# Performance work log

Hardware: AMD Instinct MI355X
Metric: run time of the kernel (lower is better)

The kernel has to match this reference:

```python
import jax, jax.numpy as jnp
import numpy as np

N_VOX = 100000   # active voxels
K = 27           # 3^3 kernel offsets
M = 60000        # matched (in, out) pairs per offset
CIN = 64
COUT = 64
BN_EPS = 1e-5


def setup_inputs() -> dict:
    key = jax.random.key(0)
    ks = jax.random.split(key, 6)
    feats = jax.random.normal(ks[0], (N_VOX, CIN), dtype=jnp.float32)
    W = jax.random.normal(ks[1], (K, CIN, COUT), dtype=jnp.float32) * 0.05
    gamma = jnp.ones((COUT,), dtype=jnp.float32)
    beta = jnp.zeros((COUT,), dtype=jnp.float32)
    running_mean = jax.random.normal(ks[2], (COUT,), dtype=jnp.float32) * 0.1
    running_var = jax.random.uniform(ks[3], (COUT,), dtype=jnp.float32, minval=0.5, maxval=1.5)
    in_idx = jax.random.randint(ks[4], (K, M), 0, N_VOX, dtype=jnp.int32)
    out_idx = jax.random.randint(ks[5], (K, M), 0, N_VOX, dtype=jnp.int32)
    return {
        "feats": feats, "W": W, "gamma": gamma, "beta": beta,
        "running_mean": running_mean, "running_var": running_var,
        "in_idx": in_idx, "out_idx": out_idx,
    }


def reference(feats, W, gamma, beta, running_mean, running_var, in_idx, out_idx):
    # Sparse conv as gather-GEMM-scatter over the hash-map kernel map.
    gathered = feats[in_idx]                              # [K, M, Cin]
    contrib = jnp.einsum('kmc,kcd->kmd', gathered, W)     # [K, M, Cout]
    out = jax.ops.segment_sum(
        contrib.reshape(-1, W.shape[-1]),                 # [K*M, Cout]
        out_idx.reshape(-1),
        num_segments=feats.shape[0],
    )                                                     # [N, Cout]
    # BatchNorm (inference, running stats) + ReLU
    inv = jax.lax.rsqrt(running_var + BN_EPS)
    y = (out - running_mean) * (inv * gamma) + beta
    return jnp.maximum(y, 0.0)
```

## Files before the change

kernel.cpp:

```cpp
#include <hip/hip_runtime.h>

#define N_VOX 100000
#define K_OFF 27
#define M_PAIR 60000
#define NPAIR (K_OFF * M_PAIR)
#define CIN 64
#define COUT 64
#define BN_EPS 1e-5f

#define VB_SHIFT 8
#define VB (1 << VB_SHIFT)
#define NB ((N_VOX + VB - 1) / VB)
#define BCAP 5120
#define PPT 16
#define PA_PAIRS (256 * PPT)
#define PA_GRID ((NPAIR + PA_PAIRS - 1) / PA_PAIRS)

#define QSPLIT 4
#define QVOX (VB / QSPLIT)
#define QCAP 1280

#define TILES_PER_WAVE 10
#define WAVES_PER_K (M_PAIR / 16 / TILES_PER_WAVE)
#define CONV_BLOCKS_X ((WAVES_PER_K + 3) / 4)

typedef __attribute__((ext_vector_type(8))) short bf16x8;
typedef __attribute__((ext_vector_type(8))) unsigned short u16x8;
typedef __attribute__((ext_vector_type(4))) unsigned int u32x4;
typedef __attribute__((ext_vector_type(4))) float f32x4;

__device__ __forceinline__ unsigned short f32_to_bf16(float f) {
    unsigned int u = __float_as_uint(f);
    u += 0x7FFFu + ((u >> 16) & 1u);
    return (unsigned short)(u >> 16);
}
__device__ __forceinline__ float bf16_lo(unsigned int u) {
    return __uint_as_float(u << 16);
}
__device__ __forceinline__ float bf16_hi(unsigned int u) {
    return __uint_as_float(u & 0xffff0000u);
}

__global__ __launch_bounds__(256) void prep_kernel(
    const float* __restrict__ feats, unsigned short* __restrict__ fb,
    const float* __restrict__ W, unsigned short* __restrict__ Wt,
    const float* __restrict__ gamma, const float* __restrict__ beta,
    const float* __restrict__ rmean, const float* __restrict__ rvar,
    float* __restrict__ bnscale, float* __restrict__ bnshift,
    int* __restrict__ bucketCount)
{
    const int gid = blockIdx.x * 256 + threadIdx.x;
    const int nt = gridDim.x * 256;
    for (int e4i = gid; e4i < (N_VOX * CIN) / 4; e4i += nt) {
        const int e4 = e4i * 4;
        const float4 v = *(const float4*)(feats + e4);
        ushort4 b;
        b.x = f32_to_bf16(v.x);
        b.y = f32_to_bf16(v.y);
        b.z = f32_to_bf16(v.z);
        b.w = f32_to_bf16(v.w);
        *(ushort4*)(fb + e4) = b;
    }
    for (int e = gid; e < K_OFF * CIN * COUT; e += nt) {
        const int k = e / (CIN * COUT);
        const int r = e % (CIN * COUT);
        Wt[k * CIN * COUT + (r % COUT) * CIN + (r / COUT)] = f32_to_bf16(W[e]);
    }
    if (gid < COUT) {
        const float inv = rsqrtf(rvar[gid] + BN_EPS);
        const float sc = inv * gamma[gid];
        bnscale[gid] = sc;
        bnshift[gid] = beta[gid] - rmean[gid] * sc;
    }
    if (gid < NB) bucketCount[gid] = 0;
}

__global__ __launch_bounds__(256) void conv_bucket_kernel(
    const unsigned short* __restrict__ fb, const unsigned short* __restrict__ Wt,
    const int* __restrict__ in_idx, const int* __restrict__ oix,
    unsigned int* __restrict__ recs, int* __restrict__ bucketCount,
    unsigned short* __restrict__ contrib)
{
    __shared__ alignas(16) unsigned short lds[4][16 * 72];
    __shared__ int lhist[NB];
    __shared__ int gbase[NB];
    const int t = threadIdx.x;
    const int k = blockIdx.y;
    const int fid = k * CONV_BLOCKS_X + blockIdx.x;

    if (fid < PA_GRID) {
        for (int i = t; i < NB; i += 256) lhist[i] = 0;
        __syncthreads();
        const int base = fid * PA_PAIRS;
        int lp[PPT];
#pragma unroll
        for (int i = 0; i < PPT; ++i) {
            const int e = base + i * 256 + t;
            lp[i] = (e < NPAIR) ? atomicAdd(&lhist[oix[e] >> VB_SHIFT], 1) : 0;
        }
        __syncthreads();
        for (int i = t; i < NB; i += 256) {
            const int c = lhist[i];
            gbase[i] = c ? atomicAdd(&bucketCount[i], c) : 0;
        }
        __syncthreads();
#pragma unroll
        for (int i = 0; i < PPT; ++i) {
            const int e = base + i * 256 + t;
            if (e < NPAIR) {
                const int v = oix[e];
                const int b = v >> VB_SHIFT;
                const int idx = gbase[b] + lp[i];
                if (idx < BCAP)
                    recs[(size_t)b * BCAP + idx] =
                        ((unsigned int)e << VB_SHIFT) | (unsigned int)(v & (VB - 1));
            }
        }
    }

    const int lane = threadIdx.x & 63;
    const int wid = threadIdx.x >> 6;
    const int w = blockIdx.x * 4 + wid;
    if (w >= WAVES_PER_K) return;
    const int col = lane & 15;
    const int quad = lane >> 4;
    unsigned short* L = lds[wid];

    bf16x8 Bf[4][2];
    const short* Wk = (const short*)(Wt + k * CIN * COUT);
#pragma unroll
    for (int tt = 0; tt < 4; ++tt) {
        const short* p = Wk + (tt * 16 + col) * CIN + quad * 8;
        Bf[tt][0] = *(const bf16x8*)(p);
        Bf[tt][1] = *(const bf16x8*)(p + 32);
    }

    int m0 = k * M_PAIR + (w * TILES_PER_WAVE) * 16;
    {
        const int rin = in_idx[m0 + col];
        const short* fp = (const short*)fb + (size_t)rin * CIN + quad * 8;
        bf16x8 A0 = *(const bf16x8*)(fp);
        bf16x8 A1 = *(const bf16x8*)(fp + 32);

        for (int it = 0; it < TILES_PER_WAVE; ++it) {
            bf16x8 nA0 = A0, nA1 = A1;
            if (it + 1 < TILES_PER_WAVE) {
                const int rn = in_idx[m0 + 16 + col];
                const short* fn = (const short*)fb + (size_t)rn * CIN + quad * 8;
                nA0 = *(const bf16x8*)(fn);
                nA1 = *(const bf16x8*)(fn + 32);
            }

            f32x4 acc[4];
#pragma unroll
            for (int tt = 0; tt < 4; ++tt) {
                f32x4 z = {0.f, 0.f, 0.f, 0.f};
                acc[tt] = __builtin_amdgcn_mfma_f32_16x16x32_bf16(A0, Bf[tt][0], z, 0, 0, 0);
                acc[tt] = __builtin_amdgcn_mfma_f32_16x16x32_bf16(A1, Bf[tt][1], acc[tt], 0, 0, 0);
            }
#pragma unroll
            for (int r = 0; r < 4; ++r) {
                const int row = quad * 4 + r;
#pragma unroll
                for (int tt = 0; tt < 4; ++tt)
                    L[row * 72 + tt * 16 + col] = f32_to_bf16(acc[tt][r]);
            }
#pragma unroll
            for (int itr = 0; itr < 2; ++itr) {
                const int row = itr * 8 + (lane >> 3);
                const int chunk = lane & 7;
                const u16x8 v = *(const u16x8*)(L + row * 72 + chunk * 8);
                *(u16x8*)(contrib + (size_t)(m0 + row) * 64 + chunk * 8) = v;
            }
            A0 = nA0;
            A1 = nA1;
            m0 += 16;
        }
    }
}

__global__ __launch_bounds__(256) void gather_bn_kernel(
    const unsigned int* __restrict__ recs, const int* __restrict__ bucketCount,
    const unsigned short* __restrict__ contrib,
    const float* __restrict__ bnscale, const float* __restrict__ bnshift,
    float* __restrict__ out)
{
    __shared__ int hist[QVOX];
    __shared__ int scan_[QVOX];
    __shared__ int cursor[QVOX];
    __shared__ int lperm[QCAP];
    __shared__ float s_sc[COUT], s_sh[COUT];
    const int blk = blockIdx.x;
    const int b = blk >> 2;
    const int q = blk & 3;
    const int t = threadIdx.x;
    if (t < QVOX) hist[t] = 0;
    if (t < COUT) { s_sc[t] = bnscale[t]; s_sh[t] = bnshift[t]; }
    __syncthreads();
    int bc = bucketCount[b];
    if (bc > BCAP) bc = BCAP;
    const unsigned int* r = recs + (size_t)b * BCAP;
    for (int i = t; i < bc; i += 256) {
        const int vl = r[i] & (VB - 1);
        if ((vl >> 6) == q) atomicAdd(&hist[vl & (QVOX - 1)], 1);
    }
    __syncthreads();
    int hc = 0;
    if (t < QVOX) { hc = hist[t]; scan_[t] = hc; }
    __syncthreads();
    for (int o = 1; o < QVOX; o <<= 1) {
        int x = (t < QVOX && t >= o) ? scan_[t - o] : 0;
        __syncthreads();
        if (t < QVOX) scan_[t] += x;
        __syncthreads();
    }
    if (t < QVOX) cursor[t] = scan_[t] - hc;
    __syncthreads();
    for (int i = t; i < bc; i += 256) {
        const unsigned int rec = r[i];
        const int vl = rec & (VB - 1);
        if ((vl >> 6) == q) {
            const int lp = atomicAdd(&cursor[vl & (QVOX - 1)], 1);
            if (lp < QCAP) lperm[lp] = (int)(rec >> VB_SHIFT);
        }
    }
    __syncthreads();
    const int wid = t >> 6;
    const int lane = t & 63;
    const int rg = lane >> 3;
    const int cg = lane & 7;
    for (int vi = wid; vi < QVOX; vi += 4) {
        const int v = b * VB + q * QVOX + vi;
        if (v >= N_VOX) continue;
        int n = hist[vi];
        const int s = scan_[vi] - n;
        if (s + n > QCAP) n = (s < QCAP) ? QCAP - s : 0;

        float a0 = 0.f, a1 = 0.f, a2 = 0.f, a3 = 0.f;
        float a4 = 0.f, a5 = 0.f, a6 = 0.f, a7 = 0.f;
        float b0 = 0.f, b1 = 0.f, b2 = 0.f, b3 = 0.f;
        float b4 = 0.f, b5 = 0.f, b6 = 0.f, b7 = 0.f;
        int j = rg;
        for (; j + 8 < n; j += 16) {
            const int p0 = lperm[s + j];
            const int p1 = lperm[s + j + 8];
            const u32x4 u = __builtin_nontemporal_load(
                (const u32x4*)(contrib + (size_t)p0 * 64) + cg);
            const u32x4 w = __builtin_nontemporal_load(
                (const u32x4*)(contrib + (size_t)p1 * 64) + cg);
            a0 += bf16_lo(u.x); a1 += bf16_hi(u.x);
            a2 += bf16_lo(u.y); a3 += bf16_hi(u.y);
            a4 += bf16_lo(u.z); a5 += bf16_hi(u.z);
            a6 += bf16_lo(u.w); a7 += bf16_hi(u.w);
            b0 += bf16_lo(w.x); b1 += bf16_hi(w.x);
            b2 += bf16_lo(w.y); b3 += bf16_hi(w.y);
            b4 += bf16_lo(w.z); b5 += bf16_hi(w.z);
            b6 += bf16_lo(w.w); b7 += bf16_hi(w.w);
        }
        for (; j < n; j += 8) {
            const int p0 = lperm[s + j];
            const u32x4 u = __builtin_nontemporal_load(
                (const u32x4*)(contrib + (size_t)p0 * 64) + cg);
            a0 += bf16_lo(u.x); a1 += bf16_hi(u.x);
            a2 += bf16_lo(u.y); a3 += bf16_hi(u.y);
            a4 += bf16_lo(u.z); a5 += bf16_hi(u.z);
            a6 += bf16_lo(u.w); a7 += bf16_hi(u.w);
        }
        a0 += b0; a1 += b1; a2 += b2; a3 += b3;
        a4 += b4; a5 += b5; a6 += b6; a7 += b7;
        a0 += __shfl_xor(a0, 8, 64); a0 += __shfl_xor(a0, 16, 64); a0 += __shfl_xor(a0, 32, 64);
        a1 += __shfl_xor(a1, 8, 64); a1 += __shfl_xor(a1, 16, 64); a1 += __shfl_xor(a1, 32, 64);
        a2 += __shfl_xor(a2, 8, 64); a2 += __shfl_xor(a2, 16, 64); a2 += __shfl_xor(a2, 32, 64);
        a3 += __shfl_xor(a3, 8, 64); a3 += __shfl_xor(a3, 16, 64); a3 += __shfl_xor(a3, 32, 64);
        a4 += __shfl_xor(a4, 8, 64); a4 += __shfl_xor(a4, 16, 64); a4 += __shfl_xor(a4, 32, 64);
        a5 += __shfl_xor(a5, 8, 64); a5 += __shfl_xor(a5, 16, 64); a5 += __shfl_xor(a5, 32, 64);
        a6 += __shfl_xor(a6, 8, 64); a6 += __shfl_xor(a6, 16, 64); a6 += __shfl_xor(a6, 32, 64);
        a7 += __shfl_xor(a7, 8, 64); a7 += __shfl_xor(a7, 16, 64); a7 += __shfl_xor(a7, 32, 64);
        if (rg == 0) {
            const int ch = cg * 8;
            float4 r0, r1;
            r0.x = fmaxf(fmaf(a0, s_sc[ch + 0], s_sh[ch + 0]), 0.f);
            r0.y = fmaxf(fmaf(a1, s_sc[ch + 1], s_sh[ch + 1]), 0.f);
            r0.z = fmaxf(fmaf(a2, s_sc[ch + 2], s_sh[ch + 2]), 0.f);
            r0.w = fmaxf(fmaf(a3, s_sc[ch + 3], s_sh[ch + 3]), 0.f);
            r1.x = fmaxf(fmaf(a4, s_sc[ch + 4], s_sh[ch + 4]), 0.f);
            r1.y = fmaxf(fmaf(a5, s_sc[ch + 5], s_sh[ch + 5]), 0.f);
            r1.z = fmaxf(fmaf(a6, s_sc[ch + 6], s_sh[ch + 6]), 0.f);
            r1.w = fmaxf(fmaf(a7, s_sc[ch + 7], s_sh[ch + 7]), 0.f);
            *(float4*)(out + (size_t)v * 64 + ch) = r0;
            *(float4*)(out + (size_t)v * 64 + ch + 4) = r1;
        }
    }
}

__global__ __launch_bounds__(256) void prep_small_kernel(
    const float* __restrict__ feats, unsigned short* __restrict__ fb,
    float* __restrict__ out, const float* __restrict__ W,
    unsigned short* __restrict__ Wt)
{
    const int e = blockIdx.x * blockDim.x + threadIdx.x;
    if (e < (N_VOX * CIN) / 4) {
        const int e4 = e * 4;
        const float4 v = *(const float4*)(feats + e4);
        ushort4 b;
        b.x = f32_to_bf16(v.x);
        b.y = f32_to_bf16(v.y);
        b.z = f32_to_bf16(v.z);
        b.w = f32_to_bf16(v.w);
        *(ushort4*)(fb + e4) = b;
        *(float4*)(out + e4) = make_float4(0.f, 0.f, 0.f, 0.f);
    }
    if (e < K_OFF * CIN * COUT) {
        const int k = e / (CIN * COUT);
        const int r = e % (CIN * COUT);
        Wt[k * CIN * COUT + (r % COUT) * CIN + (r / COUT)] = f32_to_bf16(W[e]);
    }
}

__global__ __launch_bounds__(256) void conv_atomic_kernel(
    const unsigned short* __restrict__ fb, const unsigned short* __restrict__ Wt,
    const int* __restrict__ in_idx, const int* __restrict__ out_idx,
    float* __restrict__ out)
{
    const int k = blockIdx.y;
    const int lane = threadIdx.x & 63;
    const int wave = blockIdx.x * 4 + (threadIdx.x >> 6);
    const int col = lane & 15;
    const int quad = lane >> 4;
    bf16x8 Bf[4][2];
    const short* Wk = (const short*)(Wt + k * CIN * COUT);
#pragma unroll
    for (int t = 0; t < 4; ++t) {
        const short* p = Wk + (t * 16 + col) * CIN + quad * 8;
        Bf[t][0] = *(const bf16x8*)(p);
        Bf[t][1] = *(const bf16x8*)(p + 32);
    }
    const int base = k * M_PAIR;
    for (int tile = wave; tile < M_PAIR / 16; tile += 128) {
        const int m0 = base + tile * 16;
        const int rin = in_idx[m0 + col];
        const short* fp = (const short*)fb + (size_t)rin * CIN + quad * 8;
        const bf16x8 A0 = *(const bf16x8*)(fp);
        const bf16x8 A1 = *(const bf16x8*)(fp + 32);
        f32x4 acc[4];
#pragma unroll
        for (int t = 0; t < 4; ++t) {
            f32x4 z = {0.f, 0.f, 0.f, 0.f};
            acc[t] = __builtin_amdgcn_mfma_f32_16x16x32_bf16(A0, Bf[t][0], z, 0, 0, 0);
            acc[t] = __builtin_amdgcn_mfma_f32_16x16x32_bf16(A1, Bf[t][1], acc[t], 0, 0, 0);
        }
        int vo[4];
#pragma unroll
        for (int r = 0; r < 4; ++r) vo[r] = out_idx[m0 + quad * 4 + r];
#pragma unroll
        for (int r = 0; r < 4; ++r) {
            float* op = out + (size_t)vo[r] * COUT + col;
#pragma unroll
            for (int t = 0; t < 4; ++t) atomicAdd(op + t * 16, acc[t][r]);
        }
    }
}

__global__ __launch_bounds__(256) void bn_relu_kernel(
    float* __restrict__ out,
    const float* __restrict__ gamma, const float* __restrict__ beta,
    const float* __restrict__ mean, const float* __restrict__ var)
{
    const int e = blockIdx.x * blockDim.x + threadIdx.x;
    if (e >= N_VOX * COUT) return;
    const int c = e & (COUT - 1);
    const float inv = rsqrtf(var[c] + BN_EPS);
    const float y = (out[e] - mean[c]) * (inv * gamma[c]) + beta[c];
    out[e] = fmaxf(y, 0.f);
}

extern "C" void kernel_launch(void* const* d_in, const int* in_sizes, int n_in,
                              void* d_out, int out_size, void* d_ws, size_t ws_size,
                              hipStream_t stream) {
    const float* feats = (const float*)d_in[0];
    const float* W     = (const float*)d_in[1];
    const float* gamma = (const float*)d_in[2];
    const float* beta  = (const float*)d_in[3];
    const float* rmean = (const float*)d_in[4];
    const float* rvar  = (const float*)d_in[5];
    const int* in_idx  = (const int*)d_in[6];
    const int* out_idx = (const int*)d_in[7];
    float* out = (float*)d_out;

    char* ws = (char*)d_ws;
    size_t off = 0;
    auto alloc = [&](size_t bytes) {
        size_t p = off;
        off = (off + bytes + 255) & ~(size_t)255;
        return p;
    };
    const size_t o_fb   = alloc((size_t)N_VOX * CIN * 2);
    const size_t o_wt   = alloc((size_t)K_OFF * CIN * COUT * 2);
    const size_t o_bc   = alloc((size_t)NB * 4);
    const size_t o_recs = alloc((size_t)NB * BCAP * 4);
    const size_t o_bn   = alloc((size_t)2 * COUT * 4);
    const size_t o_ctr  = alloc((size_t)NPAIR * COUT * 2);
    const bool big = (ws_size >= off);

    unsigned short* fb  = (unsigned short*)(ws + o_fb);
    unsigned short* Wt  = (unsigned short*)(ws + o_wt);
    int* bucketCount    = (int*)(ws + o_bc);
    unsigned int* recs  = (unsigned int*)(ws + o_recs);
    float* bnscale      = (float*)(ws + o_bn);
    float* bnshift      = bnscale + COUT;
    unsigned short* ctr = (unsigned short*)(ws + o_ctr);

    if (big) {
        prep_kernel<<<2048, 256, 0, stream>>>(
            feats, fb, W, Wt, gamma, beta, rmean, rvar,
            bnscale, bnshift, bucketCount);
        conv_bucket_kernel<<<dim3(CONV_BLOCKS_X, K_OFF), 256, 0, stream>>>(
            fb, Wt, in_idx, out_idx, recs, bucketCount, ctr);
        gather_bn_kernel<<<NB * QSPLIT, 256, 0, stream>>>(
            recs, bucketCount, ctr, bnscale, bnshift, out);
    } else {
        const int ptot = (N_VOX * CIN) / 4;
        prep_small_kernel<<<(ptot + 255) / 256, 256, 0, stream>>>(feats, fb, out, W, Wt);
        conv_atomic_kernel<<<dim3(32, K_OFF), 256, 0, stream>>>(fb, Wt, in_idx, out_idx, out);
        const int total_e = N_VOX * COUT;
        bn_relu_kernel<<<(total_e + 255) / 256, 256, 0, stream>>>(out, gamma, beta, rmean, rvar);
    }
}
```

Baseline: 226.4 us.

## Fuse gather-GEMM into per-bucket blocks accumulating in LDS, dropping contrib buffer

```diff
diff --git a/kernel.cpp b/kernel.cpp
--- a/kernel.cpp
+++ b/kernel.cpp
@@ -19,14 +19,9 @@
 #define QSPLIT 4
 #define QVOX (VB / QSPLIT)
 #define QCAP 1280
-
-#define TILES_PER_WAVE 10
-#define WAVES_PER_K (M_PAIR / 16 / TILES_PER_WAVE)
-#define CONV_BLOCKS_X ((WAVES_PER_K + 3) / 4)
+#define ACC_STRIDE 66
 
 typedef __attribute__((ext_vector_type(8))) short bf16x8;
-typedef __attribute__((ext_vector_type(8))) unsigned short u16x8;
-typedef __attribute__((ext_vector_type(4))) unsigned int u32x4;
 typedef __attribute__((ext_vector_type(4))) float f32x4;
 
 __device__ __forceinline__ unsigned short f32_to_bf16(float f) {
@@ -34,23 +29,57 @@
     u += 0x7FFFu + ((u >> 16) & 1u);
     return (unsigned short)(u >> 16);
 }
-__device__ __forceinline__ float bf16_lo(unsigned int u) {
-    return __uint_as_float(u << 16);
-}
-__device__ __forceinline__ float bf16_hi(unsigned int u) {
-    return __uint_as_float(u & 0xffff0000u);
-}
-
-__global__ __launch_bounds__(256) void prep_kernel(
+__device__ __forceinline__ float bf16_to_f32(unsigned short b) {
+    return __uint_as_float(((unsigned int)b) << 16);
+}
+
+__global__ __launch_bounds__(256) void prep_scatter_kernel(
+    const int* __restrict__ oix,
+    unsigned int* __restrict__ recs, int* __restrict__ bucketCount,
     const float* __restrict__ feats, unsigned short* __restrict__ fb,
-    const float* __restrict__ W, unsigned short* __restrict__ Wt,
-    const float* __restrict__ gamma, const float* __restrict__ beta,
-    const float* __restrict__ rmean, const float* __restrict__ rvar,
-    float* __restrict__ bnscale, float* __restrict__ bnshift,
-    int* __restrict__ bucketCount)
-{
-    const int gid = blockIdx.x * 256 + threadIdx.x;
-    const int nt = gridDim.x * 256;
+    const float* __restrict__ W, unsigned short* __restrict__ Wt)
+{
+    __shared__ int lhist[NB];
+    __shared__ int gbase[NB];
+    const int t = threadIdx.x;
+    for (int i = t; i < NB; i += 256) lhist[i] = 0;
+    __syncthreads();
+
+    const int base = blockIdx.x * PA_PAIRS;
+    int vsave[PPT];
+    int lpos[PPT];
+#pragma unroll
+    for (int i = 0; i < PPT; ++i) {
+        const int e = base + i * 256 + t;
+        int v = -1, lp = 0;
+        if (e < NPAIR) {
+            v = oix[e];
+            lp = atomicAdd(&lhist[v >> VB_SHIFT], 1);
+        }
+        vsave[i] = v;
+        lpos[i] = lp;
+    }
+    __syncthreads();
+    for (int i = t; i < NB; i += 256) {
+        const int c = lhist[i];
+        gbase[i] = c ? atomicAdd(&bucketCount[i], c) : 0;
+    }
+    __syncthreads();
+#pragma unroll
+    for (int i = 0; i < PPT; ++i) {
+        const int v = vsave[i];
+        if (v >= 0) {
+            const int e = base + i * 256 + t;
+            const int b = v >> VB_SHIFT;
+            const int idx = gbase[b] + lpos[i];
+            if (idx < BCAP)
+                recs[(size_t)b * BCAP + idx] =
+                    ((unsigned int)e << VB_SHIFT) | (unsigned int)(v & (VB - 1));
+        }
+    }
+
+    const int gid = blockIdx.x * 256 + t;
+    const int nt = PA_GRID * 256;
     for (int e4i = gid; e4i < (N_VOX * CIN) / 4; e4i += nt) {
         const int e4 = e4i * 4;
         const float4 v = *(const float4*)(feats + e4);
@@ -66,91 +95,96 @@
         const int r = e % (CIN * COUT);
         Wt[k * CIN * COUT + (r % COUT) * CIN + (r / COUT)] = f32_to_bf16(W[e]);
     }
-    if (gid < COUT) {
-        const float inv = rsqrtf(rvar[gid] + BN_EPS);
-        const float sc = inv * gamma[gid];
-        bnscale[gid] = sc;
-        bnshift[gid] = beta[gid] - rmean[gid] * sc;
-    }
-    if (gid < NB) bucketCount[gid] = 0;
-}
-
-__global__ __launch_bounds__(256) void conv_bucket_kernel(
+}
+
+__global__ __launch_bounds__(256) void gconv_kernel(
+    const unsigned int* __restrict__ recs, const int* __restrict__ bucketCount,
     const unsigned short* __restrict__ fb, const unsigned short* __restrict__ Wt,
-    const int* __restrict__ in_idx, const int* __restrict__ oix,
-    unsigned int* __restrict__ recs, int* __restrict__ bucketCount,
-    unsigned short* __restrict__ contrib)
-{
-    __shared__ alignas(16) unsigned short lds[4][16 * 72];
-    __shared__ int lhist[NB];
-    __shared__ int gbase[NB];
+    const int* __restrict__ in_idx,
+    const float* __restrict__ gamma, const float* __restrict__ beta,
+    const float* __restrict__ rmean, const float* __restrict__ rvar,
+    float* __restrict__ out)
+{
+    __shared__ int khist[32];
+    __shared__ int kbase[32];
+    __shared__ int kcur[32];
+    __shared__ unsigned int lpermK[QCAP];
+    __shared__ float accS[QVOX * ACC_STRIDE];
+    __shared__ float s_sc[COUT], s_sh[COUT];
+
+    const int blk = blockIdx.x;
+    const int b = blk >> 2;
+    const int q = blk & 3;
     const int t = threadIdx.x;
-    const int k = blockIdx.y;
-    const int fid = k * CONV_BLOCKS_X + blockIdx.x;
-
-    if (fid < PA_GRID) {
-        for (int i = t; i < NB; i += 256) lhist[i] = 0;
-        __syncthreads();
-        const int base = fid * PA_PAIRS;
-        int lp[PPT];
-#pragma unroll
-        for (int i = 0; i < PPT; ++i) {
-            const int e = base + i * 256 + t;
-            lp[i] = (e < NPAIR) ? atomicAdd(&lhist[oix[e] >> VB_SHIFT], 1) : 0;
-        }
-        __syncthreads();
-        for (int i = t; i < NB; i += 256) {
-            const int c = lhist[i];
-            gbase[i] = c ? atomicAdd(&bucketCount[i], c) : 0;
-        }
-        __syncthreads();
-#pragma unroll
-        for (int i = 0; i < PPT; ++i) {
-            const int e = base + i * 256 + t;
-            if (e < NPAIR) {
-                const int v = oix[e];
-                const int b = v >> VB_SHIFT;
-                const int idx = gbase[b] + lp[i];
-                if (idx < BCAP)
-                    recs[(size_t)b * BCAP + idx] =
-                        ((unsigned int)e << VB_SHIFT) | (unsigned int)(v & (VB - 1));
-            }
-        }
-    }
-
-    const int lane = threadIdx.x & 63;
-    const int wid = threadIdx.x >> 6;
-    const int w = blockIdx.x * 4 + wid;
-    if (w >= WAVES_PER_K) return;
+    if (t < 32) { khist[t] = 0; kcur[t] = 0; }
+    if (t < COUT) {
+        const float inv = rsqrtf(rvar[t] + BN_EPS);
+        const float sc = inv * gamma[t];
+        s_sc[t] = sc;
+        s_sh[t] = beta[t] - rmean[t] * sc;
+    }
+    for (int i = t; i < QVOX * ACC_STRIDE; i += 256) accS[i] = 0.f;
+    __syncthreads();
+
+    int bc = bucketCount[b];
+    if (bc > BCAP) bc = BCAP;
+    const unsigned int* r = recs + (size_t)b * BCAP;
+    for (int i = t; i < bc; i += 256) {
+        const unsigned int rec = r[i];
+        const int vl = rec & (VB - 1);
+        if ((vl >> 6) == q) atomicAdd(&khist[(rec >> VB_SHIFT) / M_PAIR], 1);
+    }
+    __syncthreads();
+    if (t == 0) {
+        int s = 0;
+        for (int k = 0; k < K_OFF; ++k) { kbase[k] = s; s += khist[k]; }
+    }
+    __syncthreads();
+    for (int i = t; i < bc; i += 256) {
+        const unsigned int rec = r[i];
+        const int vl = rec & (VB - 1);
+        if ((vl >> 6) == q) {
+            const unsigned int e = rec >> VB_SHIFT;
+            const int k = (int)(e / M_PAIR);
+            const int p = kbase[k] + atomicAdd(&kcur[k], 1);
+            if (p < QCAP)
+                lpermK[p] = ((unsigned int)(vl & 63) << 21) | e;
+        }
+    }
+    __syncthreads();
+
+    const int lane = t & 63;
+    const int wid = t >> 6;
     const int col = lane & 15;
     const int quad = lane >> 4;
-    unsigned short* L = lds[wid];
-
-    bf16x8 Bf[4][2];
-    const short* Wk = (const short*)(Wt + k * CIN * COUT);
-#pragma unroll
-    for (int tt = 0; tt < 4; ++tt) {
-        const short* p = Wk + (tt * 16 + col) * CIN + quad * 8;
-        Bf[tt][0] = *(const bf16x8*)(p);
-        Bf[tt][1] = *(const bf16x8*)(p + 32);
-    }
-
-    int m0 = k * M_PAIR + (w * TILES_PER_WAVE) * 16;
-    {
-        const int rin = in_idx[m0 + col];
-        const short* fp = (const short*)fb + (size_t)rin * CIN + quad * 8;
-        bf16x8 A0 = *(const bf16x8*)(fp);
-        bf16x8 A1 = *(const bf16x8*)(fp + 32);
-
-        for (int it = 0; it < TILES_PER_WAVE; ++it) {
-            bf16x8 nA0 = A0, nA1 = A1;
-            if (it + 1 < TILES_PER_WAVE) {
-                const int rn = in_idx[m0 + 16 + col];
-                const short* fn = (const short*)fb + (size_t)rn * CIN + quad * 8;
-                nA0 = *(const bf16x8*)(fn);
-                nA1 = *(const bf16x8*)(fn + 32);
+    for (int k = wid; k < K_OFF; k += 4) {
+        int cnt = khist[k];
+        const int base = kbase[k];
+        if (base >= QCAP) continue;
+        if (base + cnt > QCAP) cnt = QCAP - base;
+        if (cnt <= 0) continue;
+
+        bf16x8 Bf[4][2];
+        const short* Wk = (const short*)(Wt + k * CIN * COUT);
+#pragma unroll
+        for (int tt = 0; tt < 4; ++tt) {
+            const short* p = Wk + (tt * 16 + col) * CIN + quad * 8;
+            Bf[tt][0] = *(const bf16x8*)(p);
+            Bf[tt][1] = *(const bf16x8*)(p + 32);
+        }
+
+        const int ntile = (cnt + 15) >> 4;
+        for (int tile = 0; tile < ntile; ++tile) {
+            const int pr = tile * 16 + col;
+            bf16x8 A0 = {0, 0, 0, 0, 0, 0, 0, 0};
+            bf16x8 A1 = {0, 0, 0, 0, 0, 0, 0, 0};
+            if (pr < cnt) {
+                const unsigned int e = lpermK[base + pr] & 0x1FFFFFu;
+                const int rin = in_idx[e];
+                const short* fp = (const short*)fb + (size_t)rin * CIN + quad * 8;
+                A0 = *(const bf16x8*)(fp);
+                A1 = *(const bf16x8*)(fp + 32);
             }
-
             f32x4 acc[4];
 #pragma unroll
             for (int tt = 0; tt < 4; ++tt) {
@@ -159,136 +193,33 @@
                 acc[tt] = __builtin_amdgcn_mfma_f32_16x16x32_bf16(A1, Bf[tt][1], acc[tt], 0, 0, 0);
             }
 #pragma unroll
-            for (int r = 0; r < 4; ++r) {
-                const int row = quad * 4 + r;
-#pragma unroll
-                for (int tt = 0; tt < 4; ++tt)
-                    L[row * 72 + tt * 16 + col] = f32_to_bf16(acc[tt][r]);
+            for (int rr = 0; rr < 4; ++rr) {
+                const int row = tile * 16 + quad * 4 + rr;
+                if (row < cnt) {
+                    const int vl = (int)(lpermK[base + row] >> 21);
+                    float* ap = accS + vl * ACC_STRIDE + col;
+#pragma unroll
+                    for (int tt = 0; tt < 4; ++tt)
+                        atomicAdd(ap + tt * 16, acc[tt][rr]);
+                }
             }
-#pragma unroll
-            for (int itr = 0; itr < 2; ++itr) {
-                const int row = itr * 8 + (lane >> 3);
-                const int chunk = lane & 7;
-                const u16x8 v = *(const u16x8*)(L + row * 72 + chunk * 8);
-                *(u16x8*)(contrib + (size_t)(m0 + row) * 64 + chunk * 8) = v;
-            }
-            A0 = nA0;
-            A1 = nA1;
-            m0 += 16;
-        }
-    }
-}
-
-__global__ __launch_bounds__(256) void gather_bn_kernel(
-    const unsigned int* __restrict__ recs, const int* __restrict__ bucketCount,
-    const unsigned short* __restrict__ contrib,
-    const float* __restrict__ bnscale, const float* __restrict__ bnshift,
-    float* __restrict__ out)
-{
-    __shared__ int hist[QVOX];
-    __shared__ int scan_[QVOX];
-    __shared__ int cursor[QVOX];
-    __shared__ int lperm[QCAP];
-    __shared__ float s_sc[COUT], s_sh[COUT];
-    const int blk = blockIdx.x;
-    const int b = blk >> 2;
-    const int q = blk & 3;
-    const int t = threadIdx.x;
-    if (t < QVOX) hist[t] = 0;
-    if (t < COUT) { s_sc[t] = bnscale[t]; s_sh[t] = bnshift[t]; }
-    __syncthreads();
-    int bc = bucketCount[b];
-    if (bc > BCAP) bc = BCAP;
-    const unsigned int* r = recs + (size_t)b * BCAP;
-    for (int i = t; i < bc; i += 256) {
-        const int vl = r[i] & (VB - 1);
-        if ((vl >> 6) == q) atomicAdd(&hist[vl & (QVOX - 1)], 1);
-    }
-    __syncthreads();
-    int hc = 0;
-    if (t < QVOX) { hc = hist[t]; scan_[t] = hc; }
-    __syncthreads();
-    for (int o = 1; o < QVOX; o <<= 1) {
-        int x = (t < QVOX && t >= o) ? scan_[t - o] : 0;
-        __syncthreads();
-        if (t < QVOX) scan_[t] += x;
-        __syncthreads();
-    }
-    if (t < QVOX) cursor[t] = scan_[t] - hc;
-    __syncthreads();
-    for (int i = t; i < bc; i += 256) {
-        const unsigned int rec = r[i];
-        const int vl = rec & (VB - 1);
-        if ((vl >> 6) == q) {
-            const int lp = atomicAdd(&cursor[vl & (QVOX - 1)], 1);
-            if (lp < QCAP) lperm[lp] = (int)(rec >> VB_SHIFT);
-        }
-    }
-    __syncthreads();
-    const int wid = t >> 6;
-    const int lane = t & 63;
-    const int rg = lane >> 3;
-    const int cg = lane & 7;
-    for (int vi = wid; vi < QVOX; vi += 4) {
-        const int v = b * VB + q * QVOX + vi;
-        if (v >= N_VOX) continue;
-        int n = hist[vi];
-        const int s = scan_[vi] - n;
-        if (s + n > QCAP) n = (s < QCAP) ? QCAP - s : 0;
-
-        float a0 = 0.f, a1 = 0.f, a2 = 0.f, a3 = 0.f;
-        float a4 = 0.f, a5 = 0.f, a6 = 0.f, a7 = 0.f;
-        float b0 = 0.f, b1 = 0.f, b2 = 0.f, b3 = 0.f;
-        float b4 = 0.f, b5 = 0.f, b6 = 0.f, b7 = 0.f;
-        int j = rg;
-        for (; j + 8 < n; j += 16) {
-            const int p0 = lperm[s + j];
-            const int p1 = lperm[s + j + 8];
-            const u32x4 u = __builtin_nontemporal_load(
-                (const u32x4*)(contrib + (size_t)p0 * 64) + cg);
-            const u32x4 w = __builtin_nontemporal_load(
-                (const u32x4*)(contrib + (size_t)p1 * 64) + cg);
-            a0 += bf16_lo(u.x); a1 += bf16_hi(u.x);
-            a2 += bf16_lo(u.y); a3 += bf16_hi(u.y);
-            a4 += bf16_lo(u.z); a5 += bf16_hi(u.z);
-            a6 += bf16_lo(u.w); a7 += bf16_hi(u.w);
-            b0 += bf16_lo(w.x); b1 += bf16_hi(w.x);
-            b2 += bf16_lo(w.y); b3 += bf16_hi(w.y);
-            b4 += bf16_lo(w.z); b5 += bf16_hi(w.z);
-            b6 += bf16_lo(w.w); b7 += bf16_hi(w.w);
-        }
-        for (; j < n; j += 8) {
-            const int p0 = lperm[s + j];
-            const u32x4 u = __builtin_nontemporal_load(
-                (const u32x4*)(contrib + (size_t)p0 * 64) + cg);
-            a0 += bf16_lo(u.x); a1 += bf16_hi(u.x);
-            a2 += bf16_lo(u.y); a3 += bf16_hi(u.y);
-            a4 += bf16_lo(u.z); a5 += bf16_hi(u.z);
-            a6 += bf16_lo(u.w); a7 += bf16_hi(u.w);
-        }
-        a0 += b0; a1 += b1; a2 += b2; a3 += b3;
-        a4 += b4; a5 += b5; a6 += b6; a7 += b7;
-        a0 += __shfl_xor(a0, 8, 64); a0 += __shfl_xor(a0, 16, 64); a0 += __shfl_xor(a0, 32, 64);
-        a1 += __shfl_xor(a1, 8, 64); a1 += __shfl_xor(a1, 16, 64); a1 += __shfl_xor(a1, 32, 64);
-        a2 += __shfl_xor(a2, 8, 64); a2 += __shfl_xor(a2, 16, 64); a2 += __shfl_xor(a2, 32, 64);
-        a3 += __shfl_xor(a3, 8, 64); a3 += __shfl_xor(a3, 16, 64); a3 += __shfl_xor(a3, 32, 64);
-        a4 += __shfl_xor(a4, 8, 64); a4 += __shfl_xor(a4, 16, 64); a4 += __shfl_xor(a4, 32, 64);
-        a5 += __shfl_xor(a5, 8, 64); a5 += __shfl_xor(a5, 16, 64); a5 += __shfl_xor(a5, 32, 64);
-        a6 += __shfl_xor(a6, 8, 64); a6 += __shfl_xor(a6, 16, 64); a6 += __shfl_xor(a6, 32, 64);
-        a7 += __shfl_xor(a7, 8, 64); a7 += __shfl_xor(a7, 16, 64); a7 += __shfl_xor(a7, 32, 64);
-        if (rg == 0) {
-            const int ch = cg * 8;
-            float4 r0, r1;
-            r0.x = fmaxf(fmaf(a0, s_sc[ch + 0], s_sh[ch + 0]), 0.f);
-            r0.y = fmaxf(fmaf(a1, s_sc[ch + 1], s_sh[ch + 1]), 0.f);
-            r0.z = fmaxf(fmaf(a2, s_sc[ch + 2], s_sh[ch + 2]), 0.f);
-            r0.w = fmaxf(fmaf(a3, s_sc[ch + 3], s_sh[ch + 3]), 0.f);
-            r1.x = fmaxf(fmaf(a4, s_sc[ch + 4], s_sh[ch + 4]), 0.f);
-            r1.y = fmaxf(fmaf(a5, s_sc[ch + 5], s_sh[ch + 5]), 0.f);
-            r1.z = fmaxf(fmaf(a6, s_sc[ch + 6], s_sh[ch + 6]), 0.f);
-            r1.w = fmaxf(fmaf(a7, s_sc[ch + 7], s_sh[ch + 7]), 0.f);
-            *(float4*)(out + (size_t)v * 64 + ch) = r0;
-            *(float4*)(out + (size_t)v * 64 + ch + 4) = r1;
+        }
+    }
+    __syncthreads();
+
+    const int vbase = b * VB + q * QVOX;
+    for (int u = t; u < QVOX * 16; u += 256) {
+        const int vl = u >> 4;
+        const int ch = (u & 15) * 4;
+        const int v = vbase + vl;
+        if (v < N_VOX) {
+            const float* ap = accS + vl * ACC_STRIDE + ch;
+            float4 rr;
+            rr.x = fmaxf(fmaf(ap[0], s_sc[ch + 0], s_sh[ch + 0]), 0.f);
+            rr.y = fmaxf(fmaf(ap[1], s_sc[ch + 1], s_sh[ch + 1]), 0.f);
+            rr.z = fmaxf(fmaf(ap[2], s_sc[ch + 2], s_sh[ch + 2]), 0.f);
+            rr.w = fmaxf(fmaf(ap[3], s_sc[ch + 3], s_sh[ch + 3]), 0.f);
+            *(float4*)(out + (size_t)v * 64 + ch) = rr;
         }
     }
 }
@@ -398,26 +329,21 @@
     const size_t o_wt   = alloc((size_t)K_OFF * CIN * COUT * 2);
     const size_t o_bc   = alloc((size_t)NB * 4);
     const size_t o_recs = alloc((size_t)NB * BCAP * 4);
-    const size_t o_bn   = alloc((size_t)2 * COUT * 4);
-    const size_t o_ctr  = alloc((size_t)NPAIR * COUT * 2);
     const bool big = (ws_size >= off);
 
     unsigned short* fb  = (unsigned short*)(ws + o_fb);
     unsigned short* Wt  = (unsigned short*)(ws + o_wt);
     int* bucketCount    = (int*)(ws + o_bc);
     unsigned int* recs  = (unsigned int*)(ws + o_recs);
-    float* bnscale      = (float*)(ws + o_bn);
-    float* bnshift      = bnscale + COUT;
-    unsigned short* ctr = (unsigned short*)(ws + o_ctr);
 
     if (big) {
-        prep_kernel<<<2048, 256, 0, stream>>>(
-            feats, fb, W, Wt, gamma, beta, rmean, rvar,
-            bnscale, bnshift, bucketCount);
-        conv_bucket_kernel<<<dim3(CONV_BLOCKS_X, K_OFF), 256, 0, stream>>>(
-            fb, Wt, in_idx, out_idx, recs, bucketCount, ctr);
-        gather_bn_kernel<<<NB * QSPLIT, 256, 0, stream>>>(
-            recs, bucketCount, ctr, bnscale, bnshift, out);
+        hipError_t _e = hipMemsetAsync(bucketCount, 0, (size_t)NB * 4, stream);
+        (void)_e;
+        prep_scatter_kernel<<<PA_GRID, 256, 0, stream>>>(
+            out_idx, recs, bucketCount, feats, fb, W, Wt);
+        gconv_kernel<<<NB * QSPLIT, 256, 0, stream>>>(
+            recs, bucketCount, fb, Wt, in_idx,
+            gamma, beta, rmean, rvar, out);
     } else {
         const int ptot = (N_VOX * CIN) / 4;
         prep_small_kernel<<<(ptot + 255) / 256, 256, 0, stream>>>(feats, fb, out, W, Wt);
```

Measured after the change: 737.8 us. +225.9%, slower.
